# Kernel optimization log

Measured on AMD Instinct MI355X. Metric: run time of the kernel, lower is better.

The kernel has to match this reference:

```python
import jax, jax.numpy as jnp
import numpy as np

TAU = 0.1          # temperature from init_kwargs
EPS = 1e-8         # torch.nn.CosineSimilarity default eps


def setup_inputs() -> dict:
    key = jax.random.key(0)
    k1, k2, k3 = jax.random.split(key, 3)
    B, D = 2048, 128
    return {
        "z_i": jax.random.normal(k1, (B, D), dtype=jnp.float32),
        "z_j": jax.random.normal(k2, (B, D), dtype=jnp.float32),
        "y": jax.random.randint(k3, (B,), 0, 10, dtype=jnp.int64),
    }


def reference(z_i, z_j, y):
    # p: (2N, D)
    p = jnp.concatenate([z_i, z_j], axis=0)
    n2 = p.shape[0]
    # Cosine similarity via norms + single GEMM (same math as pairwise
    # CosineSimilarity: dot / max(||a||*||b||, eps)), then temperature scale.
    norms = jnp.linalg.norm(p, axis=1)                      # (2N,)
    sim = (p @ p.T) / jnp.maximum(norms[:, None] * norms[None, :], EPS) / TAU

    # Positive mask: same label, diagonal removed.
    y2 = jnp.concatenate([y, y], axis=0)                    # (2N,)
    off_diag = 1.0 - jnp.eye(n2, dtype=sim.dtype)           # logit mask
    mask = (y2[:, None] == y2[None, :]).astype(sim.dtype) * off_diag

    # Masked log-softmax over each row (self excluded from denominator).
    exp_logits = jnp.exp(sim) * off_diag
    log_prob = sim - jnp.log(exp_logits.sum(axis=1, keepdims=True))

    mean_log_prob_pos = (mask * log_prob).sum(axis=1) / mask.sum(axis=1)
    return -mean_log_prob_pos.mean()
```

## Files before the change

### kernel.cpp

```cpp
#include <hip/hip_runtime.h>

#define N2 4096
#define D 128
#define TAU_INV 10.0f
#define E2SCALE 14.4269504088896340736f
#define JSL 8
#define TPW (N2 / (JSL * 128))
#define GEMM_BLOCKS (128 * JSL)
#define NCLS 10
#define CGRP 16
#define CROWS (N2 / CGRP)
#define CB (NCLS * CGRP)

typedef __attribute__((ext_vector_type(8))) short bf16x8;
typedef __attribute__((ext_vector_type(16))) float floatx16;

__device__ __forceinline__ short f2bf(float f) {
    unsigned u = __float_as_uint(f);
    u = (u + 0x7fff + ((u >> 16) & 1)) >> 16;
    return (short)u;
}
__device__ __forceinline__ float bf2f(short s) {
    return __uint_as_float(((unsigned)(unsigned short)s) << 16);
}

__global__ __launch_bounds__(64) void prep_kernel(const float* __restrict__ zi,
                                                  const float* __restrict__ zj,
                                                  short* __restrict__ qb,
                                                  short* __restrict__ qb2,
                                                  float* __restrict__ se_g,
                                                  float* __restrict__ S) {
    int row = blockIdx.x;
    int lane = threadIdx.x;
    const float* src = (row < 2048) ? (zi + row * D) : (zj + (row - 2048) * D);
    float2 v = ((const float2*)src)[lane];
    float ss = v.x * v.x + v.y * v.y;
    #pragma unroll
    for (int m = 1; m < 64; m <<= 1) ss += __shfl_xor(ss, m);
    float inv = 1.0f / sqrtf(ss);
    short2 o;
    o.x = f2bf(v.x * inv);
    o.y = f2bf(v.y * inv);
    ((short2*)(qb + row * D))[lane] = o;
    int addr2 = (row >> 5) * 4096 + (lane >> 2) * 256 + (row & 31) * 8 + 2 * (lane & 3);
    *(short2*)(qb2 + addr2) = o;
    if (lane == 0) se_g[row] = 0.f;
    if (row == 0)
        for (int k = lane; k < NCLS * D + 2 * NCLS; k += 64) S[k] = 0.f;
}

__global__ __launch_bounds__(256) void main_kernel(const short* __restrict__ qb,
                                                   const short* __restrict__ qb2,
                                                   const long long* __restrict__ y,
                                                   float* __restrict__ se_g,
                                                   float* __restrict__ S) {
    int tid = threadIdx.x;
    int wave = tid >> 6;
    int lane = tid & 63;

    if (blockIdx.x < CB) {
        __shared__ float shS[256];
        __shared__ float shT[4];
        __shared__ float shC[2];
        int cb = blockIdx.x;
        int c  = cb / CGRP;
        int g  = cb % CGRP;
        int d  = tid & 127;
        int rh = tid >> 7;
        int r0 = g * CROWS + rh * (CROWS / 2);

        float sS = 0.f, sT = 0.f, cnt = 0.f;
        #pragma unroll 4
        for (int i = 0; i < CROWS / 2; ++i) {
            int r = r0 + i;
            bool m = ((int)y[r & 2047] == c);
            float q = bf2f(qb[r * D + d]);
            sS += m ? q : 0.f;
            sT += m ? q * q : 0.f;
            cnt += m ? 1.f : 0.f;
        }

        shS[tid] = sS;
        #pragma unroll
        for (int m = 1; m < 64; m <<= 1) sT += __shfl_xor(sT, m);
        if ((tid & 63) == 0) shT[tid >> 6] = sT;
        if (d == 0) shC[rh] = cnt;
        __syncthreads();
        if (tid < 128) atomicAdd(&S[c * D + tid], shS[tid] + shS[tid + 128]);
        if (tid == 0) {
            atomicAdd(&S[NCLS * D + c], shT[0] + shT[1] + shT[2] + shT[3]);
            atomicAdd(&S[NCLS * D + NCLS + c], shC[0] + shC[1]);
        }
        return;
    }

    int gb = blockIdx.x - CB;
    int col  = lane & 31;
    int half = lane >> 5;
    int it = gb >> 3;
    int js = gb & (JSL - 1);
    int i0 = it * 32;
    int jbase = js * (N2 / JSL);

    const short* ap = qb2 + it * 4096 + lane * 8;
    bf16x8 af[8];
    #pragma unroll
    for (int k = 0; k < 8; ++k) af[k] = *(const bf16x8*)(ap + k * 512);

    float se[16];
    #pragma unroll
    for (int r = 0; r < 16; ++r) se[r] = 0.f;

    #pragma unroll
    for (int t = 0; t < TPW; ++t) {
        int j0 = jbase + (wave + 4 * t) * 32;
        const short* bp = qb2 + (j0 >> 5) * 4096 + lane * 8;
        bf16x8 bf[8];
        #pragma unroll
        for (int k = 0; k < 8; ++k) bf[k] = *(const bf16x8*)(bp + k * 512);

        floatx16 acc;
        #pragma unroll
        for (int r = 0; r < 16; ++r) acc[r] = 0.f;
        #pragma unroll
        for (int k = 0; k < 8; ++k)
            acc = __builtin_amdgcn_mfma_f32_32x32x16_bf16(af[k], bf[k], acc, 0, 0, 0);

        if (j0 == i0) {
            int jcol = j0 + col;
            #pragma unroll
            for (int r = 0; r < 16; ++r) {
                int rowr = i0 + (r & 3) + 8 * (r >> 2) + 4 * half;
                float e = __builtin_amdgcn_exp2f(acc[r] * E2SCALE);
                se[r] += (rowr == jcol) ? 0.f : e;
            }
        } else {
            #pragma unroll
            for (int r = 0; r < 16; ++r)
                se[r] += __builtin_amdgcn_exp2f(acc[r] * E2SCALE);
        }
    }

    #pragma unroll
    for (int r = 0; r < 16; ++r) {
        float a = se[r];
        #pragma unroll
        for (int m = 1; m < 32; m <<= 1) a += __shfl_xor(a, m);
        if (col == 0) {
            int rowr = i0 + (r & 3) + 8 * (r >> 2) + 4 * half;
            atomicAdd(&se_g[rowr], a);
        }
    }
}

__global__ __launch_bounds__(256) void finish_kernel(const float* __restrict__ se_g,
                                                     const float* __restrict__ S,
                                                     float* __restrict__ out) {
    int tid = threadIdx.x;
    int wave = tid >> 6;
    int lane = tid & 63;

    float P = 0.f;
    for (int c = wave; c < NCLS; c += 4) {
        float2 sv = ((const float2*)(S + c * D))[lane];
        float s2 = sv.x * sv.x + sv.y * sv.y;
        #pragma unroll
        for (int m = 1; m < 64; m <<= 1) s2 += __shfl_xor(s2, m);
        float n = S[NCLS * D + NCLS + c];
        P += (n >= 2.0f) ? (s2 - S[NCLS * D + c]) * TAU_INV / (n - 1.0f) : 0.f;
    }

    float L = 0.f;
    for (int i = tid; i < N2; i += 256) L += __logf(se_g[i]);
    #pragma unroll
    for (int m = 1; m < 64; m <<= 1) L += __shfl_xor(L, m);

    __shared__ float red[8];
    if (lane == 0) { red[wave] = L; red[4 + wave] = P; }
    __syncthreads();
    if (tid == 0) {
        float Ls = red[0] + red[1] + red[2] + red[3];
        float Ps = red[4] + red[5] + red[6] + red[7];
        out[0] = (Ls - Ps) * (1.0f / (float)N2);
    }
}

extern "C" void kernel_launch(void* const* d_in, const int* in_sizes, int n_in,
                              void* d_out, int out_size, void* d_ws, size_t ws_size,
                              hipStream_t stream) {
    const float*     zi = (const float*)d_in[0];
    const float*     zj = (const float*)d_in[1];
    const long long* y  = (const long long*)d_in[2];
    float* out = (float*)d_out;

    char* ws = (char*)d_ws;
    short* qb   = (short*)ws;
    short* qb2  = qb + N2 * D;
    float* se_g = (float*)(ws + 2 * N2 * D * sizeof(short));
    float* S    = se_g + N2;

    prep_kernel<<<N2, 64, 0, stream>>>(zi, zj, qb, qb2, se_g, S);
    main_kernel<<<CB + GEMM_BLOCKS, 256, 0, stream>>>(qb, qb2, y, se_g, S);
    finish_kernel<<<1, 256, 0, stream>>>(se_g, S, out);
}
```

Baseline: 96.91 us.

## Retile GEMM so each wave owns its own row strip over a shared column range

Each GEMM block now covers 128 rows (four waves with 32 rows each) against a 512-column slice, with each wave looping over 16 column tiles. Previously all waves in a block shared one 32-row strip and split the columns. There are 256 GEMM blocks instead of 1024, and the GEMM blocks are placed before the class-sum blocks in the grid. The four waves now read the same B tiles, which should improve cache reuse and cut the number of atomic adds, at the cost of fewer blocks for occupancy.

After: 87.96 us. 9.2% less time.

```diff
diff --git a/kernel.cpp b/kernel.cpp
--- a/kernel.cpp
+++ b/kernel.cpp
@@ -5,8 +5,9 @@
 #define TAU_INV 10.0f
 #define E2SCALE 14.4269504088896340736f
 #define JSL 8
-#define TPW (N2 / (JSL * 128))
-#define GEMM_BLOCKS (128 * JSL)
+#define ITL 32
+#define GEMM_BLOCKS (ITL * JSL)
+#define NT 16
 #define NCLS 10
 #define CGRP 16
 #define CROWS (N2 / CGRP)
@@ -58,11 +59,11 @@
     int wave = tid >> 6;
     int lane = tid & 63;
 
-    if (blockIdx.x < CB) {
+    if (blockIdx.x >= GEMM_BLOCKS) {
         __shared__ float shS[256];
         __shared__ float shT[4];
         __shared__ float shC[2];
-        int cb = blockIdx.x;
+        int cb = blockIdx.x - GEMM_BLOCKS;
         int c  = cb / CGRP;
         int g  = cb % CGRP;
         int d  = tid & 127;
@@ -94,15 +95,15 @@
         return;
     }
 
-    int gb = blockIdx.x - CB;
+    int gb = blockIdx.x;
     int col  = lane & 31;
     int half = lane >> 5;
     int it = gb >> 3;
     int js = gb & (JSL - 1);
-    int i0 = it * 32;
-    int jbase = js * (N2 / JSL);
-
-    const short* ap = qb2 + it * 4096 + lane * 8;
+    int rbase = it * 128 + wave * 32;
+    int jbase = js * 512;
+
+    const short* ap = qb2 + ((rbase >> 5) * 4096) + lane * 8;
     bf16x8 af[8];
     #pragma unroll
     for (int k = 0; k < 8; ++k) af[k] = *(const bf16x8*)(ap + k * 512);
@@ -112,9 +113,9 @@
     for (int r = 0; r < 16; ++r) se[r] = 0.f;
 
     #pragma unroll
-    for (int t = 0; t < TPW; ++t) {
-        int j0 = jbase + (wave + 4 * t) * 32;
-        const short* bp = qb2 + (j0 >> 5) * 4096 + lane * 8;
+    for (int t = 0; t < NT; ++t) {
+        int j0 = jbase + t * 32;
+        const short* bp = qb2 + ((j0 >> 5) * 4096) + lane * 8;
         bf16x8 bf[8];
         #pragma unroll
         for (int k = 0; k < 8; ++k) bf[k] = *(const bf16x8*)(bp + k * 512);
@@ -126,11 +127,11 @@
         for (int k = 0; k < 8; ++k)
             acc = __builtin_amdgcn_mfma_f32_32x32x16_bf16(af[k], bf[k], acc, 0, 0, 0);
 
-        if (j0 == i0) {
+        if (j0 == rbase) {
             int jcol = j0 + col;
             #pragma unroll
             for (int r = 0; r < 16; ++r) {
-                int rowr = i0 + (r & 3) + 8 * (r >> 2) + 4 * half;
+                int rowr = rbase + (r & 3) + 8 * (r >> 2) + 4 * half;
                 float e = __builtin_amdgcn_exp2f(acc[r] * E2SCALE);
                 se[r] += (rowr == jcol) ? 0.f : e;
             }
@@ -147,7 +148,7 @@
         #pragma unroll
         for (int m = 1; m < 32; m <<= 1) a += __shfl_xor(a, m);
         if (col == 0) {
-            int rowr = i0 + (r & 3) + 8 * (r >> 2) + 4 * half;
+            int rowr = rbase + (r & 3) + 8 * (r >> 2) + 4 * half;
             atomicAdd(&se_g[rowr], a);
         }
     }
@@ -200,6 +201,6 @@
     float* S    = se_g + N2;
 
     prep_kernel<<<N2, 64, 0, stream>>>(zi, zj, qb, qb2, se_g, S);
-    main_kernel<<<CB + GEMM_BLOCKS, 256, 0, stream>>>(qb, qb2, y, se_g, S);
+    main_kernel<<<GEMM_BLOCKS + CB, 256, 0, stream>>>(qb, qb2, y, se_g, S);
     finish_kernel<<<1, 256, 0, stream>>>(se_g, S, out);
 }
```
